# Kernel optimization log

Hardware: AMD Instinct MI355X
Metric: run time of the kernel (lower is better)

## Reference

```python
import jax, jax.numpy as jnp
import numpy as np

D = 1024      # in_dim
HS = 64       # head_size
H = 16        # num_heads
B, S = 2, 2048


def setup_inputs() -> dict:
    key = jax.random.key(0)
    k1, k2, k3, k4, k5, k6 = jax.random.split(key, 6)
    scale = 1.0 / np.sqrt(D)
    x = jax.random.normal(k1, (B, S, D), dtype=jnp.float32)
    # Stacked per-head projection weights (torch Linear weight is [out,in];
    # random init so layout only needs to be consistent). query weight exists
    # in the torch module but is never used (source bug), so it is omitted.
    Wk = jax.random.normal(k2, (H, D, HS), dtype=jnp.float32) * scale
    Wv = jax.random.normal(k3, (H, D, HS), dtype=jnp.float32) * scale
    Wproj = jax.random.normal(k4, (H * HS, D), dtype=jnp.float32) * (1.0 / np.sqrt(H * HS))
    bproj = jax.random.normal(k5, (D,), dtype=jnp.float32) * 0.01
    return {"x": x, "Wk": Wk, "Wv": Wv, "Wproj": Wproj, "bproj": bproj}


def reference(x, Wk, Wv, Wproj, bproj):
    # Faithful to source: k = key(x); q = value(x); v = value(x)  (q == v, no softmax)
    k = jnp.einsum("bsd,hde->bhse", x, Wk)   # [B,H,S,HS]
    v = jnp.einsum("bsd,hde->bhse", x, Wv)   # [B,H,S,HS]
    q = v
    inv_sqrt = jnp.asarray(HS, x.dtype) ** -0.5
    wei = jnp.einsum("bhse,bhte->bhst", q, k) * inv_sqrt  # [B,H,S,S], unnormalized
    out = jnp.einsum("bhst,bhte->bhse", wei, v)            # [B,H,S,HS]
    # concat heads: [B,S,H*HS]
    out = jnp.transpose(out, (0, 2, 1, 3)).reshape(x.shape[0], x.shape[1], H * HS)
    return out @ Wproj + bproj  # [B,S,D]
```

## Files before the change

kernel.cpp:

```cpp
#include <hip/hip_runtime.h>

#define B_ 2
#define S_ 2048
#define D_ 1024
#define H_ 16
#define HS_ 64
#define HD_ 1024
#define SPLIT 16
#define BS_ (B_*S_)
#define BK_ 64

typedef __attribute__((ext_vector_type(8))) short short8_t;
typedef __attribute__((ext_vector_type(8))) unsigned short ushort8_t;
typedef __attribute__((ext_vector_type(4))) float float4_t;

__device__ inline unsigned short f32_to_bf16(float f) {
  unsigned int u = __float_as_uint(f);
  u += 0x7FFF + ((u >> 16) & 1);
  return (unsigned short)(u >> 16);
}
__device__ inline float bf16_to_f32(unsigned short s) {
  return __uint_as_float(((unsigned int)s) << 16);
}

__device__ inline void async_copy16(const void* g, void* lds) {
  __builtin_amdgcn_global_load_lds(
      (const __attribute__((address_space(1))) void*)g,
      (__attribute__((address_space(3))) void*)lds, 16, 0, 0);
}


__global__ __launch_bounds__(256) void prep_kernel(
    const float* __restrict__ x, const float* __restrict__ Wk,
    const float* __restrict__ Wv, unsigned short* __restrict__ xb,
    unsigned short* __restrict__ Wkvt) {
  const int blk = blockIdx.x;
  const int tid = threadIdx.x;
  __shared__ float lds[64][65];
  if (blk < 4096) {
    int idx = blk * 256 + tid;
    float4 v = ((const float4*)x)[idx];
    ushort4 o;
    o.x = f32_to_bf16(v.x); o.y = f32_to_bf16(v.y);
    o.z = f32_to_bf16(v.z); o.w = f32_to_bf16(v.w);
    ((ushort4*)xb)[idx] = o;
    return;
  }
  const int wblk = blk - 4096;
  const int h = wblk >> 4;
  const int d0 = (wblk & 15) * 64;
#pragma unroll
  for (int i = 0; i < 16; ++i) {
    int idx = tid + i * 256; int dd = idx >> 6, e = idx & 63;
    lds[e][dd] = Wk[((size_t)h * D_ + d0 + dd) * HS_ + e];
  }
  __syncthreads();
#pragma unroll
  for (int i = 0; i < 16; ++i) {
    int idx = tid + i * 256; int e = idx >> 6, dd = idx & 63;
    Wkvt[((size_t)h * 128 + e) * D_ + d0 + dd] = f32_to_bf16(lds[e][dd]);
  }
  __syncthreads();
#pragma unroll
  for (int i = 0; i < 16; ++i) {
    int idx = tid + i * 256; int dd = idx >> 6, e = idx & 63;
    lds[e][dd] = Wv[((size_t)h * D_ + d0 + dd) * HS_ + e];
  }
  __syncthreads();
#pragma unroll
  for (int i = 0; i < 16; ++i) {
    int idx = tid + i * 256; int e = idx >> 6, dd = idx & 63;
    Wkvt[((size_t)h * 128 + 64 + e) * D_ + d0 + dd] = f32_to_bf16(lds[e][dd]);
  }
}

__global__ __launch_bounds__(256) void kv_mfma_kernel(
    const unsigned short* __restrict__ xb,
    const unsigned short* __restrict__ Wkvt,
    unsigned short* __restrict__ Kb,
    unsigned short* __restrict__ Vb) {
  const int blk = blockIdx.x;
  const int stile = blk & 31;
  const int h = blk >> 5;
  const int s0 = stile * 128;
  const int tid = threadIdx.x;
  const int lane = tid & 63;
  const int wid = tid >> 6;
  const int wm = wid & 1, wn = wid >> 1;
  const int quad = lane >> 4, l16 = lane & 15;
  const int srow8 = lane >> 3;
  const int csw = ((lane & 7) ^ srow8) * 8;
  const int xa = l16 & 7;

  __shared__ __align__(16) unsigned short As[128 * BK_];
  __shared__ __align__(16) unsigned short Bs[128 * BK_];

  float4_t acc[4][4];
  const float4_t fz = {0.f, 0.f, 0.f, 0.f};
#pragma unroll
  for (int i = 0; i < 4; ++i)
#pragma unroll
    for (int j = 0; j < 4; ++j) acc[i][j] = fz;

  for (int k0 = 0; k0 < D_; k0 += BK_) {
#pragma unroll
    for (int i = 0; i < 4; ++i) {
      int g = wid * 4 + i;
      int r = g * 8 + srow8;
      async_copy16(xb + (size_t)(s0 + r) * D_ + k0 + csw, As + g * 8 * BK_);
      async_copy16(Wkvt + ((size_t)h * 128 + r) * D_ + k0 + csw, Bs + g * 8 * BK_);
    }
    __syncthreads();
    short8_t a[4][2], b[4][2];
#pragma unroll
    for (int mi = 0; mi < 4; ++mi)
#pragma unroll
      for (int ks = 0; ks < 2; ++ks)
        a[mi][ks] = *(const short8_t*)(As + (wm * 64 + mi * 16 + l16) * BK_ +
                                       ((ks * 4 + quad) ^ xa) * 8);
#pragma unroll
    for (int ni = 0; ni < 4; ++ni)
#pragma unroll
      for (int ks = 0; ks < 2; ++ks)
        b[ni][ks] = *(const short8_t*)(Bs + (wn * 64 + ni * 16 + l16) * BK_ +
                                       ((ks * 4 + quad) ^ xa) * 8);
#pragma unroll
    for (int ks = 0; ks < 2; ++ks)
#pragma unroll
      for (int mi = 0; mi < 4; ++mi)
#pragma unroll
        for (int ni = 0; ni < 4; ++ni)
          acc[mi][ni] = __builtin_amdgcn_mfma_f32_16x16x32_bf16(
              a[mi][ks], b[ni][ks], acc[mi][ni], 0, 0, 0);
    __syncthreads();
  }
  unsigned short* dst = (wn == 0) ? Kb : Vb;
#pragma unroll
  for (int mi = 0; mi < 4; ++mi)
#pragma unroll
    for (int ni = 0; ni < 4; ++ni) {
      int c = h * 64 + ni * 16 + l16;
      int rowb = s0 + wm * 64 + mi * 16 + quad * 4;
#pragma unroll
      for (int r = 0; r < 4; ++r)
        dst[(size_t)(rowb + r) * HD_ + c] = f32_to_bf16(acc[mi][ni][r]);
    }
}

__global__ __launch_bounds__(256) void m_partial_kernel(
    const unsigned short* __restrict__ Kb, const unsigned short* __restrict__ Vb,
    float* __restrict__ Mpart) {
  const int blk = blockIdx.x;
  const int h = blk & 15;
  const int b = (blk >> 4) & 1;
  const int split = blk >> 5;
  const int tid = threadIdx.x;
  const int tx = tid & 15, ty = tid >> 4;
  __shared__ float Ks[64][68];
  __shared__ float Vs[64][68];
  float acc[4][4] = {};
  const int sBase = split * (S_ / SPLIT);
  for (int sc = 0; sc < S_ / SPLIT; sc += 64) {
#pragma unroll
    for (int i = 0; i < 2; ++i) {
      int ch = tid + i * 256;
      int r = ch >> 3, c = (ch & 7) * 8;
      size_t g = (size_t)(b * S_ + sBase + sc + r) * HD_ + h * HS_ + c;
      ushort8_t k8 = *(const ushort8_t*)(Kb + g);
      ushort8_t v8 = *(const ushort8_t*)(Vb + g);
#pragma unroll
      for (int j = 0; j < 8; ++j) {
        Ks[r][c + j] = bf16_to_f32(k8[j]);
        Vs[r][c + j] = bf16_to_f32(v8[j]);
      }
    }
    __syncthreads();
#pragma unroll
    for (int ss = 0; ss < 64; ++ss) {
      const float4 a4 = *(const float4*)&Ks[ss][ty * 4];
      const float4 b4 = *(const float4*)&Vs[ss][tx * 4];
      const float a[4] = {a4.x, a4.y, a4.z, a4.w};
      const float bb[4] = {b4.x, b4.y, b4.z, b4.w};
#pragma unroll
      for (int i = 0; i < 4; ++i)
#pragma unroll
        for (int j = 0; j < 4; ++j) acc[i][j] += a[i] * bb[j];
    }
    __syncthreads();
  }
  float* dst = Mpart + ((size_t)(split * B_ + b) * H_ + h) * HS_ * HS_;
#pragma unroll
  for (int i = 0; i < 4; ++i) {
    float4 o = {acc[i][0], acc[i][1], acc[i][2], acc[i][3]};
    *(float4*)&dst[(ty * 4 + i) * HS_ + tx * 4] = o;
  }
}

__global__ __launch_bounds__(256) void m_reduce_kernel(
    const float* __restrict__ Mpart, float* __restrict__ M) {
  const int gid = blockIdx.x * 256 + threadIdx.x;
  const int e0 = gid * 4;
  const int bh = e0 >> 12;
  const int idx = e0 & 4095;
  float4 s = {0.f, 0.f, 0.f, 0.f};
#pragma unroll
  for (int p = 0; p < SPLIT; ++p) {
    const float4 v = *(const float4*)&Mpart[((size_t)(p * B_ * H_) + bh) * 4096 + idx];
    s.x += v.x; s.y += v.y; s.z += v.z; s.w += v.w;
  }
  s.x *= 0.125f; s.y *= 0.125f; s.z *= 0.125f; s.w *= 0.125f;
  *(float4*)&M[(size_t)bh * 4096 + idx] = s;
}

__global__ __launch_bounds__(256) void p_kernel(
    const float* __restrict__ M, const float* __restrict__ Wproj,
    unsigned short* __restrict__ Pt) {
  const int blk = blockIdx.x;
  const int dtile = blk & 15;
  const int h = (blk >> 4) & 15;
  const int b = blk >> 8;
  const int d0 = dtile * 64;
  const int tid = threadIdx.x;
  const int tx = tid & 15, ty = tid >> 4;
  __shared__ float Ms[64][68];
  __shared__ float Ws[64][68];
  const size_t mbase = ((size_t)(b * H_ + h)) * HS_ * HS_;
#pragma unroll
  for (int i = 0; i < 16; ++i) {
    int idx = tid + i * 256;
    int f = idx >> 6, e = idx & 63;
    Ms[e][f] = M[mbase + idx];
    Ws[f][e] = Wproj[(size_t)(h * HS_ + f) * D_ + d0 + e];
  }
  __syncthreads();
  float acc[4][4] = {};
#pragma unroll
  for (int kk = 0; kk < 64; ++kk) {
    const float4 a4 = *(const float4*)&Ms[kk][ty * 4];
    const float4 b4 = *(const float4*)&Ws[kk][tx * 4];
    const float a[4] = {a4.x, a4.y, a4.z, a4.w};
    const float bb[4] = {b4.x, b4.y, b4.z, b4.w};
#pragma unroll
    for (int i = 0; i < 4; ++i)
#pragma unroll
      for (int j = 0; j < 4; ++j) acc[i][j] += a[i] * bb[j];
  }
  __syncthreads();
#pragma unroll
  for (int i = 0; i < 4; ++i)
#pragma unroll
    for (int j = 0; j < 4; ++j)
      Ms[tx * 4 + j][ty * 4 + i] = acc[i][j];
  __syncthreads();
  {
    int c = tid >> 2, ch = tid & 3;
    unsigned short* dst = Pt + ((size_t)(b * D_ + d0 + c)) * HD_ + h * 64 + ch * 16;
#pragma unroll
    for (int e = 0; e < 16; ++e) dst[e] = f32_to_bf16(Ms[c][ch * 16 + e]);
  }
}

__global__ __launch_bounds__(256) void out_mfma_kernel(
    const unsigned short* __restrict__ Vb,
    const unsigned short* __restrict__ Pt,
    const float* __restrict__ bproj,
    float* __restrict__ out) {
  const int blk = blockIdx.x;
  const int ntile = blk & 15;
  const int stile = blk >> 4;
  const int s0 = stile * 128;
  const int n0 = ntile * 64;
  const int b = s0 >> 11;
  const int tid = threadIdx.x;
  const int lane = tid & 63;
  const int wid = tid >> 6;
  const int wm = wid & 1, wn = wid >> 1;
  const int quad = lane >> 4, l16 = lane & 15;
  const int srow8 = lane >> 3;
  const int csw = ((lane & 7) ^ srow8) * 8;
  const int xa = l16 & 7;

  __shared__ __align__(16) unsigned short As[128 * BK_];
  __shared__ __align__(16) unsigned short Bs[64 * BK_];

  float4_t acc[4][2];
  const float4_t fz = {0.f, 0.f, 0.f, 0.f};
#pragma unroll
  for (int i = 0; i < 4; ++i)
#pragma unroll
    for (int j = 0; j < 2; ++j) acc[i][j] = fz;

  const unsigned short* Bpanel = Pt + (size_t)b * D_ * HD_;
  for (int k0 = 0; k0 < HD_; k0 += BK_) {
#pragma unroll
    for (int i = 0; i < 4; ++i) {
      int g = wid * 4 + i;
      int r = g * 8 + srow8;
      async_copy16(Vb + (size_t)(s0 + r) * HD_ + k0 + csw, As + g * 8 * BK_);
    }
#pragma unroll
    for (int i = 0; i < 2; ++i) {
      int g = wid * 2 + i;
      int r = g * 8 + srow8;
      async_copy16(Bpanel + (size_t)(n0 + r) * HD_ + k0 + csw, Bs + g * 8 * BK_);
    }
    __syncthreads();
    short8_t a[4][2], bfr[2][2];
#pragma unroll
    for (int mi = 0; mi < 4; ++mi)
#pragma unroll
      for (int ks = 0; ks < 2; ++ks)
        a[mi][ks] = *(const short8_t*)(As + (wm * 64 + mi * 16 + l16) * BK_ +
                                       ((ks * 4 + quad) ^ xa) * 8);
#pragma unroll
    for (int ni = 0; ni < 2; ++ni)
#pragma unroll
      for (int ks = 0; ks < 2; ++ks)
        bfr[ni][ks] = *(const short8_t*)(Bs + (wn * 32 + ni * 16 + l16) * BK_ +
                                         ((ks * 4 + quad) ^ xa) * 8);
#pragma unroll
    for (int ks = 0; ks < 2; ++ks)
#pragma unroll
      for (int mi = 0; mi < 4; ++mi)
#pragma unroll
        for (int ni = 0; ni < 2; ++ni)
          acc[mi][ni] = __builtin_amdgcn_mfma_f32_16x16x32_bf16(
              a[mi][ks], bfr[ni][ks], acc[mi][ni], 0, 0, 0);
    __syncthreads();
  }
#pragma unroll
  for (int ni = 0; ni < 2; ++ni) {
    int col = n0 + wn * 32 + ni * 16 + l16;
    float bias = bproj[col];
#pragma unroll
    for (int mi = 0; mi < 4; ++mi) {
      int rowb = s0 + wm * 64 + mi * 16 + quad * 4;
#pragma unroll
      for (int r = 0; r < 4; ++r)
        out[(size_t)(rowb + r) * D_ + col] = acc[mi][ni][r] + bias;
    }
  }
}

extern "C" void kernel_launch(void* const* d_in, const int* in_sizes, int n_in,
                              void* d_out, int out_size, void* d_ws, size_t ws_size,
                              hipStream_t stream) {
  const float* x = (const float*)d_in[0];
  const float* Wk = (const float*)d_in[1];
  const float* Wv = (const float*)d_in[2];
  const float* Wproj = (const float*)d_in[3];
  const float* bproj = (const float*)d_in[4];
  float* out = (float*)d_out;

  char* ws = (char*)d_ws;
  unsigned short* xb = (unsigned short*)ws;
  unsigned short* Wkvt = xb + (size_t)BS_ * D_;
  unsigned short* Kb = Wkvt + (size_t)H_ * 128 * D_;
  unsigned short* Vb = Kb + (size_t)BS_ * HD_;
  float* Mpart = (float*)(Vb + (size_t)BS_ * HD_);
  float* M = Mpart + (size_t)SPLIT * B_ * H_ * HS_ * HS_;
  unsigned short* Pt = (unsigned short*)(M + (size_t)B_ * H_ * HS_ * HS_);

  prep_kernel<<<dim3(4096 + H_ * (D_ / 64)), dim3(256), 0, stream>>>(x, Wk, Wv, xb, Wkvt);
  kv_mfma_kernel<<<dim3((BS_ / 128) * H_), dim3(256), 0, stream>>>(xb, Wkvt, Kb, Vb);
  m_partial_kernel<<<dim3(SPLIT * B_ * H_), dim3(256), 0, stream>>>(Kb, Vb, Mpart);
  m_reduce_kernel<<<dim3(128), dim3(256), 0, stream>>>(Mpart, M);
  p_kernel<<<dim3(B_ * H_ * (D_ / 64)), dim3(256), 0, stream>>>(M, Wproj, Pt);
  out_mfma_kernel<<<dim3((BS_ / 128) * (D_ / 64)), dim3(256), 0, stream>>>(Vb, Pt, bproj, out);
}
```

Measured before the change: 145.1 us.

## Use MFMA for K^T V partials with transposed K/V layout, split KV tiles

The K/V projection kernel now writes K and V transposed (feature-major) alongside row-major V, and is split into twice as many blocks, each covering half the 128 output columns. The K^T·V partial-product kernel is rewritten from scalar FP32 FMA with LDS staging into a single-wave bf16 MFMA kernel that reads the transposed operands straight from global memory. The output GEMM doubles its K-tile to 128 with a reworked swizzle to halve barrier count. This adds extra global writes for the transposed copies, and the partial kernel now does its products with bf16 MFMA in place of FP32 FMAs.

```diff
diff --git a/kernel.cpp b/kernel.cpp
--- a/kernel.cpp
+++ b/kernel.cpp
@@ -9,18 +9,15 @@
 #define SPLIT 16
 #define BS_ (B_*S_)
 #define BK_ 64
+#define BKO_ 128
 
 typedef __attribute__((ext_vector_type(8))) short short8_t;
-typedef __attribute__((ext_vector_type(8))) unsigned short ushort8_t;
 typedef __attribute__((ext_vector_type(4))) float float4_t;
 
 __device__ inline unsigned short f32_to_bf16(float f) {
   unsigned int u = __float_as_uint(f);
   u += 0x7FFF + ((u >> 16) & 1);
   return (unsigned short)(u >> 16);
-}
-__device__ inline float bf16_to_f32(unsigned short s) {
-  return __uint_as_float(((unsigned int)s) << 16);
 }
 
 __device__ inline void async_copy16(const void* g, void* lds) {
@@ -74,126 +71,139 @@
   }
 }
 
-__global__ __launch_bounds__(256) void kv_mfma_kernel(
+__global__ __launch_bounds__(256, 4) void kv_mfma_kernel(
     const unsigned short* __restrict__ xb,
     const unsigned short* __restrict__ Wkvt,
-    unsigned short* __restrict__ Kb,
-    unsigned short* __restrict__ Vb) {
+    unsigned short* __restrict__ Kt,
+    unsigned short* __restrict__ Vb,
+    unsigned short* __restrict__ Vt) {
   const int blk = blockIdx.x;
   const int stile = blk & 31;
-  const int h = blk >> 5;
+  const int ntile = blk >> 5;
+  const int h = ntile >> 1, half = ntile & 1;
   const int s0 = stile * 128;
   const int tid = threadIdx.x;
   const int lane = tid & 63;
   const int wid = tid >> 6;
-  const int wm = wid & 1, wn = wid >> 1;
   const int quad = lane >> 4, l16 = lane & 15;
   const int srow8 = lane >> 3;
   const int csw = ((lane & 7) ^ srow8) * 8;
   const int xa = l16 & 7;
 
   __shared__ __align__(16) unsigned short As[128 * BK_];
-  __shared__ __align__(16) unsigned short Bs[128 * BK_];
-
-  float4_t acc[4][4];
+  __shared__ __align__(16) unsigned short Bs[64 * BK_];
+
+  float4_t acc[2][4];
   const float4_t fz = {0.f, 0.f, 0.f, 0.f};
 #pragma unroll
-  for (int i = 0; i < 4; ++i)
+  for (int i = 0; i < 2; ++i)
 #pragma unroll
     for (int j = 0; j < 4; ++j) acc[i][j] = fz;
 
+  const unsigned short* Brow = Wkvt + ((size_t)h * 128 + half * 64) * D_;
   for (int k0 = 0; k0 < D_; k0 += BK_) {
 #pragma unroll
     for (int i = 0; i < 4; ++i) {
       int g = wid * 4 + i;
       int r = g * 8 + srow8;
       async_copy16(xb + (size_t)(s0 + r) * D_ + k0 + csw, As + g * 8 * BK_);
-      async_copy16(Wkvt + ((size_t)h * 128 + r) * D_ + k0 + csw, Bs + g * 8 * BK_);
+    }
+#pragma unroll
+    for (int i = 0; i < 2; ++i) {
+      int g = wid * 2 + i;
+      int r = g * 8 + srow8;
+      async_copy16(Brow + (size_t)r * D_ + k0 + csw, Bs + g * 8 * BK_);
     }
     __syncthreads();
-    short8_t a[4][2], b[4][2];
-#pragma unroll
-    for (int mi = 0; mi < 4; ++mi)
+    short8_t a[2][2], b[4][2];
+#pragma unroll
+    for (int mi = 0; mi < 2; ++mi)
 #pragma unroll
       for (int ks = 0; ks < 2; ++ks)
-        a[mi][ks] = *(const short8_t*)(As + (wm * 64 + mi * 16 + l16) * BK_ +
+        a[mi][ks] = *(const short8_t*)(As + (wid * 32 + mi * 16 + l16) * BK_ +
                                        ((ks * 4 + quad) ^ xa) * 8);
 #pragma unroll
     for (int ni = 0; ni < 4; ++ni)
 #pragma unroll
       for (int ks = 0; ks < 2; ++ks)
-        b[ni][ks] = *(const short8_t*)(Bs + (wn * 64 + ni * 16 + l16) * BK_ +
+        b[ni][ks] = *(const short8_t*)(Bs + (ni * 16 + l16) * BK_ +
                                        ((ks * 4 + quad) ^ xa) * 8);
 #pragma unroll
     for (int ks = 0; ks < 2; ++ks)
 #pragma unroll
-      for (int mi = 0; mi < 4; ++mi)
+      for (int mi = 0; mi < 2; ++mi)
 #pragma unroll
         for (int ni = 0; ni < 4; ++ni)
           acc[mi][ni] = __builtin_amdgcn_mfma_f32_16x16x32_bf16(
               a[mi][ks], b[ni][ks], acc[mi][ni], 0, 0, 0);
     __syncthreads();
   }
-  unsigned short* dst = (wn == 0) ? Kb : Vb;
-#pragma unroll
-  for (int mi = 0; mi < 4; ++mi)
+#pragma unroll
+  for (int mi = 0; mi < 2; ++mi)
 #pragma unroll
     for (int ni = 0; ni < 4; ++ni) {
-      int c = h * 64 + ni * 16 + l16;
-      int rowb = s0 + wm * 64 + mi * 16 + quad * 4;
-#pragma unroll
-      for (int r = 0; r < 4; ++r)
-        dst[(size_t)(rowb + r) * HD_ + c] = f32_to_bf16(acc[mi][ni][r]);
-    }
-}
-
-__global__ __launch_bounds__(256) void m_partial_kernel(
-    const unsigned short* __restrict__ Kb, const unsigned short* __restrict__ Vb,
+      int fr = h * 64 + ni * 16 + l16;
+      int sc = s0 + wid * 32 + mi * 16 + quad * 4;
+      ushort4 o;
+      o.x = f32_to_bf16(acc[mi][ni][0]);
+      o.y = f32_to_bf16(acc[mi][ni][1]);
+      o.z = f32_to_bf16(acc[mi][ni][2]);
+      o.w = f32_to_bf16(acc[mi][ni][3]);
+      if (half == 0) {
+        *(ushort4*)&Kt[(size_t)fr * BS_ + sc] = o;
+      } else {
+        *(ushort4*)&Vt[(size_t)fr * BS_ + sc] = o;
+#pragma unroll
+        for (int r = 0; r < 4; ++r)
+          Vb[(size_t)(sc + r) * HD_ + fr] = ((const unsigned short*)&o)[r];
+      }
+    }
+}
+
+__global__ __launch_bounds__(64) void m_partial_kernel(
+    const unsigned short* __restrict__ Kt, const unsigned short* __restrict__ Vt,
     float* __restrict__ Mpart) {
   const int blk = blockIdx.x;
   const int h = blk & 15;
   const int b = (blk >> 4) & 1;
   const int split = blk >> 5;
-  const int tid = threadIdx.x;
-  const int tx = tid & 15, ty = tid >> 4;
-  __shared__ float Ks[64][68];
-  __shared__ float Vs[64][68];
-  float acc[4][4] = {};
-  const int sBase = split * (S_ / SPLIT);
-  for (int sc = 0; sc < S_ / SPLIT; sc += 64) {
-#pragma unroll
-    for (int i = 0; i < 2; ++i) {
-      int ch = tid + i * 256;
-      int r = ch >> 3, c = (ch & 7) * 8;
-      size_t g = (size_t)(b * S_ + sBase + sc + r) * HD_ + h * HS_ + c;
-      ushort8_t k8 = *(const ushort8_t*)(Kb + g);
-      ushort8_t v8 = *(const ushort8_t*)(Vb + g);
-#pragma unroll
-      for (int j = 0; j < 8; ++j) {
-        Ks[r][c + j] = bf16_to_f32(k8[j]);
-        Vs[r][c + j] = bf16_to_f32(v8[j]);
-      }
-    }
-    __syncthreads();
-#pragma unroll
-    for (int ss = 0; ss < 64; ++ss) {
-      const float4 a4 = *(const float4*)&Ks[ss][ty * 4];
-      const float4 b4 = *(const float4*)&Vs[ss][tx * 4];
-      const float a[4] = {a4.x, a4.y, a4.z, a4.w};
-      const float bb[4] = {b4.x, b4.y, b4.z, b4.w};
-#pragma unroll
-      for (int i = 0; i < 4; ++i)
-#pragma unroll
-        for (int j = 0; j < 4; ++j) acc[i][j] += a[i] * bb[j];
-    }
-    __syncthreads();
-  }
-  float* dst = Mpart + ((size_t)(split * B_ + b) * H_ + h) * HS_ * HS_;
-#pragma unroll
-  for (int i = 0; i < 4; ++i) {
-    float4 o = {acc[i][0], acc[i][1], acc[i][2], acc[i][3]};
-    *(float4*)&dst[(ty * 4 + i) * HS_ + tx * 4] = o;
-  }
+  const int lane = threadIdx.x;
+  const int quad = lane >> 4, l16 = lane & 15;
+  const int sBase = b * S_ + split * (S_ / SPLIT);
+
+  const unsigned short* Krow = Kt + (size_t)h * 64 * BS_;
+  const unsigned short* Vrow = Vt + (size_t)h * 64 * BS_;
+
+  float4_t acc[4][4];
+  const float4_t fz = {0.f, 0.f, 0.f, 0.f};
+#pragma unroll
+  for (int i = 0; i < 4; ++i)
+#pragma unroll
+    for (int j = 0; j < 4; ++j) acc[i][j] = fz;
+
+  for (int sc = 0; sc < S_ / SPLIT; sc += 32) {
+    short8_t a[4], bfr[4];
+#pragma unroll
+    for (int mi = 0; mi < 4; ++mi)
+      a[mi] = *(const short8_t*)&Krow[(size_t)(mi * 16 + l16) * BS_ + sBase + sc + quad * 8];
+#pragma unroll
+    for (int ni = 0; ni < 4; ++ni)
+      bfr[ni] = *(const short8_t*)&Vrow[(size_t)(ni * 16 + l16) * BS_ + sBase + sc + quad * 8];
+#pragma unroll
+    for (int mi = 0; mi < 4; ++mi)
+#pragma unroll
+      for (int ni = 0; ni < 4; ++ni)
+        acc[mi][ni] = __builtin_amdgcn_mfma_f32_16x16x32_bf16(
+            a[mi], bfr[ni], acc[mi][ni], 0, 0, 0);
+  }
+  float* dst = Mpart + (((size_t)split * B_ + b) * H_ + h) * 4096;
+#pragma unroll
+  for (int mi = 0; mi < 4; ++mi)
+#pragma unroll
+    for (int ni = 0; ni < 4; ++ni)
+#pragma unroll
+      for (int r = 0; r < 4; ++r)
+        dst[(mi * 16 + quad * 4 + r) * 64 + ni * 16 + l16] = acc[mi][ni][r];
 }
 
 __global__ __launch_bounds__(256) void m_reduce_kernel(
@@ -276,12 +286,11 @@
   const int wid = tid >> 6;
   const int wm = wid & 1, wn = wid >> 1;
   const int quad = lane >> 4, l16 = lane & 15;
-  const int srow8 = lane >> 3;
-  const int csw = ((lane & 7) ^ srow8) * 8;
+  const int srow4 = lane >> 4;
   const int xa = l16 & 7;
 
-  __shared__ __align__(16) unsigned short As[128 * BK_];
-  __shared__ __align__(16) unsigned short Bs[64 * BK_];
+  __shared__ __align__(16) unsigned short As[128 * BKO_];
+  __shared__ __align__(16) unsigned short Bs[64 * BKO_];
 
   float4_t acc[4][2];
   const float4_t fz = {0.f, 0.f, 0.f, 0.f};
@@ -291,35 +300,37 @@
     for (int j = 0; j < 2; ++j) acc[i][j] = fz;
 
   const unsigned short* Bpanel = Pt + (size_t)b * D_ * HD_;
-  for (int k0 = 0; k0 < HD_; k0 += BK_) {
+  for (int k0 = 0; k0 < HD_; k0 += BKO_) {
+#pragma unroll
+    for (int i = 0; i < 8; ++i) {
+      int g = wid * 8 + i;
+      int r = g * 4 + srow4;
+      int ch = (l16 ^ (r & 7)) * 8;
+      async_copy16(Vb + (size_t)(s0 + r) * HD_ + k0 + ch, As + g * 4 * BKO_);
+    }
 #pragma unroll
     for (int i = 0; i < 4; ++i) {
       int g = wid * 4 + i;
-      int r = g * 8 + srow8;
-      async_copy16(Vb + (size_t)(s0 + r) * HD_ + k0 + csw, As + g * 8 * BK_);
-    }
-#pragma unroll
-    for (int i = 0; i < 2; ++i) {
-      int g = wid * 2 + i;
-      int r = g * 8 + srow8;
-      async_copy16(Bpanel + (size_t)(n0 + r) * HD_ + k0 + csw, Bs + g * 8 * BK_);
+      int r = g * 4 + srow4;
+      int ch = (l16 ^ (r & 7)) * 8;
+      async_copy16(Bpanel + (size_t)(n0 + r) * HD_ + k0 + ch, Bs + g * 4 * BKO_);
     }
     __syncthreads();
-    short8_t a[4][2], bfr[2][2];
+    short8_t a[4][4], bfr[2][4];
 #pragma unroll
     for (int mi = 0; mi < 4; ++mi)
 #pragma unroll
-      for (int ks = 0; ks < 2; ++ks)
-        a[mi][ks] = *(const short8_t*)(As + (wm * 64 + mi * 16 + l16) * BK_ +
+      for (int ks = 0; ks < 4; ++ks)
+        a[mi][ks] = *(const short8_t*)(As + (wm * 64 + mi * 16 + l16) * BKO_ +
                                        ((ks * 4 + quad) ^ xa) * 8);
 #pragma unroll
     for (int ni = 0; ni < 2; ++ni)
 #pragma unroll
-      for (int ks = 0; ks < 2; ++ks)
-        bfr[ni][ks] = *(const short8_t*)(Bs + (wn * 32 + ni * 16 + l16) * BK_ +
+      for (int ks = 0; ks < 4; ++ks)
+        bfr[ni][ks] = *(const short8_t*)(Bs + (wn * 32 + ni * 16 + l16) * BKO_ +
                                          ((ks * 4 + quad) ^ xa) * 8);
 #pragma unroll
-    for (int ks = 0; ks < 2; ++ks)
+    for (int ks = 0; ks < 4; ++ks)
 #pragma unroll
       for (int mi = 0; mi < 4; ++mi)
 #pragma unroll
@@ -355,16 +366,17 @@
   char* ws = (char*)d_ws;
   unsigned short* xb = (unsigned short*)ws;
   unsigned short* Wkvt = xb + (size_t)BS_ * D_;
-  unsigned short* Kb = Wkvt + (size_t)H_ * 128 * D_;
-  unsigned short* Vb = Kb + (size_t)BS_ * HD_;
-  float* Mpart = (float*)(Vb + (size_t)BS_ * HD_);
+  unsigned short* Kt = Wkvt + (size_t)H_ * 128 * D_;
+  unsigned short* Vb = Kt + (size_t)HD_ * BS_;
+  unsigned short* Vt = Vb + (size_t)BS_ * HD_;
+  float* Mpart = (float*)(Vt + (size_t)HD_ * BS_);
   float* M = Mpart + (size_t)SPLIT * B_ * H_ * HS_ * HS_;
   unsigned short* Pt = (unsigned short*)(M + (size_t)B_ * H_ * HS_ * HS_);
 
   prep_kernel<<<dim3(4096 + H_ * (D_ / 64)), dim3(256), 0, stream>>>(x, Wk, Wv, xb, Wkvt);
-  kv_mfma_kernel<<<dim3((BS_ / 128) * H_), dim3(256), 0, stream>>>(xb, Wkvt, Kb, Vb);
-  m_partial_kernel<<<dim3(SPLIT * B_ * H_), dim3(256), 0, stream>>>(Kb, Vb, Mpart);
+  kv_mfma_kernel<<<dim3(32 * 32), dim3(256), 0, stream>>>(xb, Wkvt, Kt, Vb, Vt);
+  m_partial_kernel<<<dim3(SPLIT * B_ * H_), dim3(64), 0, stream>>>(Kt, Vt, Mpart);
   m_reduce_kernel<<<dim3(128), dim3(256), 0, stream>>>(Mpart, M);
   p_kernel<<<dim3(B_ * H_ * (D_ / 64)), dim3(256), 0, stream>>>(M, Wproj, Pt);
-  out_mfma_kernel<<<dim3((BS_ / 128) * (D_ / 64)), dim3(256), 0, stream>>>(Vb, Pt, bproj, out);
-}
+  out_mfma_kernel<<<dim3(32 * 16), dim3(256), 0, stream>>>(Vb, Pt, bproj, out);
+}
```

New measurement: 139.5 us. 1.04x faster.
